# Performance work log

Measured on AMD Instinct MI355X. Metric: run time of the kernel, lower is better.

Reference implementation:

```python
import jax, jax.numpy as jnp
import numpy as np

B, S, IN, OUT = 4, 2048, 4096, 11008

def setup_inputs() -> dict:
    key = jax.random.key(0)
    k1, k2, k3, k4, k5 = jax.random.split(key, 5)
    x = jax.random.normal(k1, (B, S, IN), dtype=jnp.float32)
    weight_4bit = jax.random.randint(k2, (OUT, IN), 0, 16, dtype=jnp.int32)
    # per-tensor scalar scale / zero_point, stored with shape [1] like the torch buffers
    scale = jax.random.uniform(k3, (1,), dtype=jnp.float32, minval=0.001, maxval=0.01)
    zero_point = jnp.round(jax.random.uniform(k4, (1,), dtype=jnp.float32, minval=0.0, maxval=15.0))
    bias = jax.random.normal(k5, (OUT,), dtype=jnp.float32) * 0.01
    return {"x": x, "weight_4bit": weight_4bit, "scale": scale, "zero_point": zero_point, "bias": bias}

def reference(x, weight_4bit, scale, zero_point, bias):
    # dequantize: w_rec = (w_q - zero_point) * scale, shape [OUT, IN]
    w = (weight_4bit.astype(jnp.float32) - zero_point) * scale
    # out[b,s,o] = sum_i x[b,s,i] * w[o,i] + bias[o]
    out = jnp.einsum('bsi,oi->bso', x, w) + bias
    return out
```

## Files before the change

### kernel.cpp

```cpp
#include <hip/hip_runtime.h>
#include <cstdint>
#include <cstddef>

#define Mdim 8192
#define Ndim 11008
#define Kdim 4096
#define BM 128
#define BN 128
#define BK 64
#define GROUP_M 16

typedef __attribute__((ext_vector_type(8))) __bf16 bf16x8;
typedef __attribute__((ext_vector_type(4))) float floatx4;

__device__ inline unsigned f2bf(float f) {
    union { float f; unsigned u; } v; v.f = f;
    unsigned r = v.u + 0x7fffu + ((v.u >> 16) & 1u);
    return r >> 16;
}
__device__ inline unsigned pack2(float lo, float hi) {
    return f2bf(lo) | (f2bf(hi) << 16);
}

__global__ void cvt_x_kernel(const float4* __restrict__ x, uint4* __restrict__ o, int n8) {
    int i = blockIdx.x * blockDim.x + threadIdx.x;
    if (i >= n8) return;
    float4 a = x[2 * i];
    float4 b = x[2 * i + 1];
    uint4 r;
    r.x = pack2(a.x, a.y);
    r.y = pack2(a.z, a.w);
    r.z = pack2(b.x, b.y);
    r.w = pack2(b.z, b.w);
    o[i] = r;
}

__global__ void cvt_w_kernel(const int4* __restrict__ w, uint4* __restrict__ o,
                             const float* __restrict__ scale, const float* __restrict__ zp,
                             int n8) {
    int i = blockIdx.x * blockDim.x + threadIdx.x;
    if (i >= n8) return;
    float s = scale[0];
    float z = zp[0];
    int4 a = w[2 * i];
    int4 b = w[2 * i + 1];
    uint4 r;
    r.x = pack2(((float)a.x - z) * s, ((float)a.y - z) * s);
    r.y = pack2(((float)a.z - z) * s, ((float)a.w - z) * s);
    r.z = pack2(((float)b.x - z) * s, ((float)b.y - z) * s);
    r.w = pack2(((float)b.z - z) * s, ((float)b.w - z) * s);
    o[i] = r;
}

__global__ __launch_bounds__(256) void gemm_kernel(const short* __restrict__ A,
                                                   const short* __restrict__ B,
                                                   const float* __restrict__ bias,
                                                   float* __restrict__ C) {
    __shared__ __align__(16) short As[BM * BK];
    __shared__ __align__(16) short Bs[BN * BK];

    const int tid  = threadIdx.x;
    const int lane = tid & 63;
    const int wave = tid >> 6;
    const int waveM = wave >> 1;
    const int waveN = wave & 1;
    const int l15  = lane & 15;
    const int quad = lane >> 4;

    const int NT = Ndim / BN;
    int pid   = blockIdx.x;
    int group = pid / (GROUP_M * NT);
    int rem   = pid % (GROUP_M * NT);
    int mt    = group * GROUP_M + (rem % GROUP_M);
    int nt    = rem / GROUP_M;
    const int mBase = mt * BM;
    const int nBase = nt * BN;

    floatx4 acc[4][4];
    #pragma unroll
    for (int i = 0; i < 4; ++i)
        #pragma unroll
        for (int j = 0; j < 4; ++j)
            acc[i][j] = (floatx4)0.0f;

    const short* ga[4];
    const short* gb[4];
    int ldsoff[4];
    #pragma unroll
    for (int r = 0; r < 4; ++r) {
        int li  = r * 256 + tid;
        int row = li >> 3;
        int pc  = li & 7;
        int gc  = pc ^ (row & 7);
        ga[r] = A + (size_t)(mBase + row) * Kdim + gc * 8;
        gb[r] = B + (size_t)(nBase + row) * Kdim + gc * 8;
        ldsoff[r] = li * 8;
    }

    for (int k0 = 0; k0 < Kdim; k0 += BK) {
        #pragma unroll
        for (int r = 0; r < 4; ++r)
            __builtin_amdgcn_global_load_lds(
                (const __attribute__((address_space(1))) void*)(ga[r] + k0),
                (__attribute__((address_space(3))) void*)(As + ldsoff[r]), 16, 0, 0);
        #pragma unroll
        for (int r = 0; r < 4; ++r)
            __builtin_amdgcn_global_load_lds(
                (const __attribute__((address_space(1))) void*)(gb[r] + k0),
                (__attribute__((address_space(3))) void*)(Bs + ldsoff[r]), 16, 0, 0);
        __syncthreads();

        #pragma unroll
        for (int kk = 0; kk < 2; ++kk) {
            bf16x8 af[4], bfr[4];
            const int c = kk * 4 + quad;
            #pragma unroll
            for (int i = 0; i < 4; ++i) {
                int rowA = waveM * 64 + i * 16 + l15;
                af[i]  = *(const bf16x8*)(As + (rowA * 8 + (c ^ (rowA & 7))) * 8);
                int rowB = waveN * 64 + i * 16 + l15;
                bfr[i] = *(const bf16x8*)(Bs + (rowB * 8 + (c ^ (rowB & 7))) * 8);
            }
            #pragma unroll
            for (int i = 0; i < 4; ++i)
                #pragma unroll
                for (int j = 0; j < 4; ++j)
                    acc[i][j] = __builtin_amdgcn_mfma_f32_16x16x32_bf16(
                        af[i], bfr[j], acc[i][j], 0, 0, 0);
        }
        __syncthreads();
    }

    #pragma unroll
    for (int j = 0; j < 4; ++j) {
        int col = nBase + waveN * 64 + j * 16 + l15;
        float bv = bias[col];
        #pragma unroll
        for (int i = 0; i < 4; ++i) {
            int row0 = mBase + waveM * 64 + i * 16 + quad * 4;
            #pragma unroll
            for (int r = 0; r < 4; ++r)
                C[(size_t)(row0 + r) * Ndim + col] = acc[i][j][r] + bv;
        }
    }
}

extern "C" void kernel_launch(void* const* d_in, const int* in_sizes, int n_in,
                              void* d_out, int out_size, void* d_ws, size_t ws_size,
                              hipStream_t stream) {
    const float* x     = (const float*)d_in[0];
    const int*   w4    = (const int*)  d_in[1];
    const float* scale = (const float*)d_in[2];
    const float* zp    = (const float*)d_in[3];
    const float* bias  = (const float*)d_in[4];
    float* out = (float*)d_out;

    short* Abf = (short*)d_ws;
    short* Wbf = Abf + (size_t)Mdim * Kdim;

    const int nx8 = Mdim * Kdim / 8;
    cvt_x_kernel<<<nx8 / 256, 256, 0, stream>>>((const float4*)x, (uint4*)Abf, nx8);

    const int nw8 = Ndim * Kdim / 8;
    cvt_w_kernel<<<nw8 / 256, 256, 0, stream>>>((const int4*)w4, (uint4*)Wbf, scale, zp, nw8);

    const int nblocks = (Ndim / BN) * (Mdim / BM);
    gemm_kernel<<<nblocks, 256, 0, stream>>>(Abf, Wbf, bias, out);
}
```

Measured before the change: 1.297 ms.

## Use 256x256 tiles with a 4-stage LDS pipeline and 8-wave blocks

Enlarges the GEMM block tile to 256x256 with BK=32 and 512 threads, so each wave computes a 128x64 sub-tile. Global-to-LDS loads are issued three k-steps ahead into a 4-buffer ring, with explicit vmcnt waits and raw barriers. Each k-step is split into two MFMA halves, with s_setprio raised around the MFMA runs. The aim is to hide memory latency and raise arithmetic intensity per LDS byte. The cost is 128KB of LDS and higher register pressure, which limits occupancy to about one block per CU.

```diff
diff --git a/kernel.cpp b/kernel.cpp
--- a/kernel.cpp
+++ b/kernel.cpp
@@ -5,9 +5,12 @@
 #define Mdim 8192
 #define Ndim 11008
 #define Kdim 4096
-#define BM 128
-#define BN 128
-#define BK 64
+#define BM 256
+#define BN 256
+#define BK 32
+#define NK (Kdim / BK)
+#define NBUF 4
+#define TILE_ELEMS (BM * BK)
 #define GROUP_M 16
 
 typedef __attribute__((ext_vector_type(8))) __bf16 bf16x8;
@@ -52,23 +55,24 @@
     o[i] = r;
 }
 
-__global__ __launch_bounds__(256) void gemm_kernel(const short* __restrict__ A,
-                                                   const short* __restrict__ B,
-                                                   const float* __restrict__ bias,
-                                                   float* __restrict__ C) {
-    __shared__ __align__(16) short As[BM * BK];
-    __shared__ __align__(16) short Bs[BN * BK];
-
-    const int tid  = threadIdx.x;
-    const int lane = tid & 63;
-    const int wave = tid >> 6;
-    const int waveM = wave >> 1;
-    const int waveN = wave & 1;
-    const int l15  = lane & 15;
-    const int quad = lane >> 4;
+__global__ __launch_bounds__(512, 2) void gemm_kernel(const short* __restrict__ A,
+                                                      const short* __restrict__ B,
+                                                      const float* __restrict__ bias,
+                                                      float* __restrict__ C) {
+    __shared__ __align__(16) short As[NBUF][TILE_ELEMS];
+    __shared__ __align__(16) short Bs[NBUF][TILE_ELEMS];
+
+    const int tid   = threadIdx.x;
+    const int lane  = tid & 63;
+    const int wave  = tid >> 6;
+    const int waveM = wave >> 2;
+    const int waveN = wave & 3;
+    const int l15   = lane & 15;
+    const int quad  = lane >> 4;
 
     const int NT = Ndim / BN;
     int pid   = blockIdx.x;
+    if (pid >= (Ndim / BN) * (Mdim / BM)) return;
     int group = pid / (GROUP_M * NT);
     int rem   = pid % (GROUP_M * NT);
     int mt    = group * GROUP_M + (rem % GROUP_M);
@@ -76,68 +80,107 @@
     const int mBase = mt * BM;
     const int nBase = nt * BN;
 
-    floatx4 acc[4][4];
+    floatx4 acc[8][4];
     #pragma unroll
-    for (int i = 0; i < 4; ++i)
+    for (int i = 0; i < 8; ++i)
         #pragma unroll
         for (int j = 0; j < 4; ++j)
             acc[i][j] = (floatx4)0.0f;
 
-    const short* ga[4];
-    const short* gb[4];
-    int ldsoff[4];
-    #pragma unroll
-    for (int r = 0; r < 4; ++r) {
-        int li  = r * 256 + tid;
-        int row = li >> 3;
-        int pc  = li & 7;
-        int gc  = pc ^ (row & 7);
-        ga[r] = A + (size_t)(mBase + row) * Kdim + gc * 8;
-        gb[r] = B + (size_t)(nBase + row) * Kdim + gc * 8;
-        ldsoff[r] = li * 8;
+    const int srow = tid >> 2;
+    const int spc  = tid & 3;
+    const int sgc  = spc ^ ((srow >> 1) & 3);
+    const short* gA0 = A + (size_t)(mBase + srow) * Kdim + sgc * 8;
+    const short* gA1 = gA0 + (size_t)128 * Kdim;
+    const short* gB0 = B + (size_t)(nBase + srow) * Kdim + sgc * 8;
+    const short* gB1 = gB0 + (size_t)128 * Kdim;
+    const int ld0 = tid * 8;
+    const int ld1 = ld0 + 4096;
+
+    const int pch  = (l15 >> 1) & 3;
+    const int qa   = (quad ^ pch) * 8;
+    const int aoff = (waveM * 128 + l15) * BK + qa;
+    const int boff = (waveN * 64  + l15) * BK + qa;
+
+#define FENCE() asm volatile("" ::: "memory")
+#define BAR()   do { FENCE(); __builtin_amdgcn_s_barrier(); FENCE(); } while (0)
+
+#define GLL(SRC, DST) __builtin_amdgcn_global_load_lds(                        \
+        (const __attribute__((address_space(1))) void*)(SRC),                  \
+        (__attribute__((address_space(3))) void*)(DST), 16, 0, 0)
+
+#define STAGE_A(KT) do {                                                       \
+        GLL(gA0 + (KT) * BK, &As[(KT) & 3][ld0]);                              \
+        GLL(gA1 + (KT) * BK, &As[(KT) & 3][ld1]);                              \
+    } while (0)
+#define STAGE_B(KT) do {                                                       \
+        GLL(gB0 + (KT) * BK, &Bs[(KT) & 3][ld0]);                              \
+        GLL(gB1 + (KT) * BK, &Bs[(KT) & 3][ld1]);                              \
+    } while (0)
+
+#define MFMA_ROW(II, AV) do {                                                              \
+        acc[II][0] = __builtin_amdgcn_mfma_f32_16x16x32_bf16(AV, b0, acc[II][0], 0, 0, 0); \
+        acc[II][1] = __builtin_amdgcn_mfma_f32_16x16x32_bf16(AV, b1, acc[II][1], 0, 0, 0); \
+        acc[II][2] = __builtin_amdgcn_mfma_f32_16x16x32_bf16(AV, b2, acc[II][2], 0, 0, 0); \
+        acc[II][3] = __builtin_amdgcn_mfma_f32_16x16x32_bf16(AV, b3, acc[II][3], 0, 0, 0); \
+    } while (0)
+
+#define KBODY(T, DOSTAGE) do {                                                 \
+        const int bi_ = (T) & 3;                                               \
+        const short* ab_ = &As[bi_][aoff];                                     \
+        const short* bb_ = &Bs[bi_][boff];                                     \
+        bf16x8 b0 = *(const bf16x8*)(bb_ + 0 * 512);                           \
+        bf16x8 b1 = *(const bf16x8*)(bb_ + 1 * 512);                           \
+        bf16x8 b2 = *(const bf16x8*)(bb_ + 2 * 512);                           \
+        bf16x8 b3 = *(const bf16x8*)(bb_ + 3 * 512);                           \
+        bf16x8 a0 = *(const bf16x8*)(ab_ + 0 * 512);                           \
+        bf16x8 a1 = *(const bf16x8*)(ab_ + 1 * 512);                           \
+        bf16x8 a2 = *(const bf16x8*)(ab_ + 2 * 512);                           \
+        bf16x8 a3 = *(const bf16x8*)(ab_ + 3 * 512);                           \
+        if (DOSTAGE) { STAGE_A((T) + 3); }                                     \
+        BAR();                                                                 \
+        __builtin_amdgcn_s_setprio(1);                                         \
+        MFMA_ROW(0, a0); MFMA_ROW(1, a1); MFMA_ROW(2, a2); MFMA_ROW(3, a3);    \
+        __builtin_amdgcn_s_setprio(0);                                         \
+        BAR();                                                                 \
+        bf16x8 a4 = *(const bf16x8*)(ab_ + 4 * 512);                           \
+        bf16x8 a5 = *(const bf16x8*)(ab_ + 5 * 512);                           \
+        bf16x8 a6 = *(const bf16x8*)(ab_ + 6 * 512);                           \
+        bf16x8 a7 = *(const bf16x8*)(ab_ + 7 * 512);                           \
+        if (DOSTAGE) { STAGE_B((T) + 3); }                                     \
+        BAR();                                                                 \
+        __builtin_amdgcn_s_setprio(1);                                         \
+        MFMA_ROW(4, a4); MFMA_ROW(5, a5); MFMA_ROW(6, a6); MFMA_ROW(7, a7);    \
+        __builtin_amdgcn_s_setprio(0);                                         \
+    } while (0)
+
+    STAGE_A(0); STAGE_B(0);
+    STAGE_A(1); STAGE_B(1);
+    STAGE_A(2); STAGE_B(2);
+    asm volatile("s_waitcnt vmcnt(8)" ::: "memory");
+    BAR();
+
+    #pragma unroll 1
+    for (int t = 0; t < NK - 3; ++t) {
+        KBODY(t, 1);
+        asm volatile("s_waitcnt vmcnt(8)" ::: "memory");
+        BAR();
     }
-
-    for (int k0 = 0; k0 < Kdim; k0 += BK) {
-        #pragma unroll
-        for (int r = 0; r < 4; ++r)
-            __builtin_amdgcn_global_load_lds(
-                (const __attribute__((address_space(1))) void*)(ga[r] + k0),
-                (__attribute__((address_space(3))) void*)(As + ldsoff[r]), 16, 0, 0);
-        #pragma unroll
-        for (int r = 0; r < 4; ++r)
-            __builtin_amdgcn_global_load_lds(
-                (const __attribute__((address_space(1))) void*)(gb[r] + k0),
-                (__attribute__((address_space(3))) void*)(Bs + ldsoff[r]), 16, 0, 0);
-        __syncthreads();
-
-        #pragma unroll
-        for (int kk = 0; kk < 2; ++kk) {
-            bf16x8 af[4], bfr[4];
-            const int c = kk * 4 + quad;
-            #pragma unroll
-            for (int i = 0; i < 4; ++i) {
-                int rowA = waveM * 64 + i * 16 + l15;
-                af[i]  = *(const bf16x8*)(As + (rowA * 8 + (c ^ (rowA & 7))) * 8);
-                int rowB = waveN * 64 + i * 16 + l15;
-                bfr[i] = *(const bf16x8*)(Bs + (rowB * 8 + (c ^ (rowB & 7))) * 8);
-            }
-            #pragma unroll
-            for (int i = 0; i < 4; ++i)
-                #pragma unroll
-                for (int j = 0; j < 4; ++j)
-                    acc[i][j] = __builtin_amdgcn_mfma_f32_16x16x32_bf16(
-                        af[i], bfr[j], acc[i][j], 0, 0, 0);
-        }
-        __syncthreads();
-    }
+    KBODY(NK - 3, 0);
+    asm volatile("s_waitcnt vmcnt(4)" ::: "memory");
+    BAR();
+    KBODY(NK - 2, 0);
+    asm volatile("s_waitcnt vmcnt(0)" ::: "memory");
+    BAR();
+    KBODY(NK - 1, 0);
 
     #pragma unroll
     for (int j = 0; j < 4; ++j) {
         int col = nBase + waveN * 64 + j * 16 + l15;
         float bv = bias[col];
         #pragma unroll
-        for (int i = 0; i < 4; ++i) {
-            int row0 = mBase + waveM * 64 + i * 16 + quad * 4;
+        for (int i = 0; i < 8; ++i) {
+            int row0 = mBase + waveM * 128 + i * 16 + quad * 4;
             #pragma unroll
             for (int r = 0; r < 4; ++r)
                 C[(size_t)(row0 + r) * Ndim + col] = acc[i][j][r] + bv;
@@ -165,5 +208,5 @@
     cvt_w_kernel<<<nw8 / 256, 256, 0, stream>>>((const int4*)w4, (uint4*)Wbf, scale, zp, nw8);
 
     const int nblocks = (Ndim / BN) * (Mdim / BM);
-    gemm_kernel<<<nblocks, 256, 0, stream>>>(Abf, Wbf, bias, out);
-}
+    gemm_kernel<<<nblocks, 512, 0, stream>>>(Abf, Wbf, bias, out);
+}
```

Result: slower. 1.467 ms (+13.2%).
